# Optimization experiments

Hardware: AMD Instinct MI355X
Metric: run time of the kernel (lower is better)

The kernel has to match this reference:

```python
import jax, jax.numpy as jnp
import numpy as np

D_MODEL = 1024
NUM_HEADS = 16

def setup_inputs() -> dict:
    key = jax.random.key(0)
    k1, k2, k3 = jax.random.split(key, 3)
    scale = 1.0 / np.sqrt(D_MODEL)
    x = jax.random.normal(k1, (2, 2048, D_MODEL), dtype=jnp.float32)
    Wqkv = jax.random.normal(k2, (D_MODEL, 3 * D_MODEL), dtype=jnp.float32) * scale
    bqkv = jnp.zeros((3 * D_MODEL,), dtype=jnp.float32)
    Wout = jax.random.normal(k3, (D_MODEL, D_MODEL), dtype=jnp.float32) * scale
    bout = jnp.zeros((D_MODEL,), dtype=jnp.float32)
    return {"x": x, "Wqkv": Wqkv, "bqkv": bqkv, "Wout": Wout, "bout": bout}

def reference(x, Wqkv, bqkv, Wout, bout):
    B, T, d_model = x.shape
    H = NUM_HEADS
    d_k = d_model // H
    qkv = x @ Wqkv + bqkv                         # [B, T, 3*d_model]
    q, k, v = jnp.split(qkv, 3, axis=-1)
    def reshape(t):
        return t.reshape(B, T, H, d_k).transpose(0, 2, 1, 3)  # [B, H, T, d_k]
    q, k, v = map(reshape, (q, k, v))
    scores = jnp.einsum("bhqd,bhkd->bhqk", q, k) / jnp.sqrt(jnp.float32(d_k))
    attn = jax.nn.softmax(scores, axis=-1)        # [B, H, T, T]
    out = jnp.einsum("bhqk,bhkd->bhqd", attn, v)  # [B, H, T, d_k]
    out = out.transpose(0, 2, 1, 3).reshape(B, T, d_model)
    return out @ Wout + bout
```

## Files before the change

kernel.cpp:

```cpp
#include <hip/hip_runtime.h>
#include <stdint.h>

#define D_MODEL 1024
#define T_SEQ   2048
#define BATCH   2
#define NHEAD   16
#define DK      64

typedef short s16x8 __attribute__((ext_vector_type(8)));
typedef float f32x4 __attribute__((ext_vector_type(4)));
typedef float f32x16 __attribute__((ext_vector_type(16)));

#define MFMA16(a, b, c) __builtin_amdgcn_mfma_f32_16x16x32_bf16((a), (b), (c), 0, 0, 0)
#define MFMA32(a, b, c) __builtin_amdgcn_mfma_f32_32x32x16_bf16((a), (b), (c), 0, 0, 0)
#define CROW(r) ((((r) & 3)) + 8 * ((r) >> 2))

__device__ __forceinline__ unsigned short f2bf(float f) {
    union { float f; unsigned u; } v; v.f = f;
    unsigned r = v.u + 0x7fffu + ((v.u >> 16) & 1u);
    return (unsigned short)(r >> 16);
}

__device__ __forceinline__ unsigned cvtpk_bf16(float lo, float hi) {
    unsigned r;
    asm("v_cvt_pk_bf16_f32 %0, %1, %2" : "=v"(r) : "v"(lo), "v"(hi));
    return r;
}

__device__ __forceinline__ float exp2a(float x) {
    float r;
    asm("v_exp_f32 %0, %1" : "=v"(r) : "v"(x));
    return r;
}

__device__ __forceinline__ float bperm_f(int srclane, float v) {
    int iv = __builtin_bit_cast(int, v);
    int r = __builtin_amdgcn_ds_bpermute(srclane << 2, iv);
    return __builtin_bit_cast(float, r);
}

__global__ __launch_bounds__(256) void cast_x(const float* __restrict__ in,
                                              unsigned short* __restrict__ out, int n8) {
    int i = blockIdx.x * 256 + threadIdx.x;
    if (i >= n8) return;
    const float4* p = reinterpret_cast<const float4*>(in) + (size_t)i * 2;
    float4 a = p[0], b = p[1];
    union { s16x8 v; unsigned short u[8]; } o;
    o.u[0] = f2bf(a.x); o.u[1] = f2bf(a.y); o.u[2] = f2bf(a.z); o.u[3] = f2bf(a.w);
    o.u[4] = f2bf(b.x); o.u[5] = f2bf(b.y); o.u[6] = f2bf(b.z); o.u[7] = f2bf(b.w);
    reinterpret_cast<s16x8*>(out)[i] = o.v;
}

__global__ __launch_bounds__(256) void transpose_cast(const float* __restrict__ in,
                                                      unsigned short* __restrict__ out,
                                                      int R, int C) {
    __shared__ unsigned short tile[64][66];
    int c0 = blockIdx.x * 64, r0 = blockIdx.y * 64;
    int tid = threadIdx.x;
#pragma unroll
    for (int i = 0; i < 16; ++i) {
        int idx = tid + i * 256;
        int r = idx >> 6, c = idx & 63;
        tile[r][c] = f2bf(in[(size_t)(r0 + r) * C + c0 + c]);
    }
    __syncthreads();
#pragma unroll
    for (int i = 0; i < 16; ++i) {
        int idx = tid + i * 256;
        int cc = idx >> 6, rr = idx & 63;
        out[(size_t)(c0 + cc) * R + r0 + rr] = tile[rr][cc];
    }
}

__global__ __launch_bounds__(256) void transpose_v(const unsigned short* __restrict__ in,
                                                   unsigned short* __restrict__ out) {
    __shared__ unsigned short tile[64][66];
    int t0 = blockIdx.x * 64, bh = blockIdx.y;
    int tid = threadIdx.x;
    const unsigned short* src = in + (size_t)bh * T_SEQ * DK;
    unsigned short* dst = out + (size_t)bh * DK * T_SEQ;
#pragma unroll
    for (int i = 0; i < 16; ++i) {
        int idx = tid + i * 256;
        int tr = idx >> 6, d = idx & 63;
        tile[tr][d] = src[(size_t)(t0 + tr) * DK + d];
    }
    __syncthreads();
#pragma unroll
    for (int i = 0; i < 16; ++i) {
        int idx = tid + i * 256;
        int dd = idx >> 6, tt = idx & 63;
        dst[(size_t)dd * T_SEQ + t0 + tt] = tile[tt][dd];
    }
}

__device__ __forceinline__ void gload_lds16(const void* g, void* l) {
    __builtin_amdgcn_global_load_lds(
        (const __attribute__((address_space(1))) void*)g,
        (__attribute__((address_space(3))) void*)l, 16, 0, 0);
}

template <int EPI>
__global__ __launch_bounds__(256) void gemm_bt(
    const unsigned short* __restrict__ A, const unsigned short* __restrict__ Bt,
    int K, int N, const float* __restrict__ bias,
    float* __restrict__ outF,
    unsigned short* __restrict__ Qw, unsigned short* __restrict__ Kw,
    unsigned short* __restrict__ Vw) {
    __shared__ __align__(16) unsigned short lds[2][8192];
    const int tid = threadIdx.x;
    const int lane = tid & 63, wid = tid >> 6;
    const int g = lane >> 4, l15 = lane & 15;
    const int wm = wid >> 1, wn = wid & 1;
    const int mTile = blockIdx.y, nTile = blockIdx.x;
    const unsigned short* Ab = A + (size_t)mTile * 128 * K;
    const unsigned short* Bb = Bt + (size_t)nTile * 128 * K;
    const int srow = tid >> 2, schunk = (tid & 3) * 8;
    f32x4 acc[4][4] = {};

    auto stage = [&](int buf, int kt) {
        const unsigned short* ga = Ab + (size_t)srow * K + kt * 32 + schunk;
        const unsigned short* gb = Bb + (size_t)srow * K + kt * 32 + schunk;
        unsigned short* la = &lds[buf][tid * 8];
        unsigned short* lb = &lds[buf][4096 + tid * 8];
        gload_lds16(ga, la);
        gload_lds16(ga + (size_t)64 * K, la + 2048);
        gload_lds16(gb, lb);
        gload_lds16(gb + (size_t)64 * K, lb + 2048);
    };

    stage(0, 0);
    __syncthreads();
    const int nk = K >> 5;
    int buf = 0;
    for (int kt = 0; kt < nk; ++kt) {
        if (kt + 1 < nk) stage(buf ^ 1, kt + 1);
        const unsigned short* la = &lds[buf][0];
        const unsigned short* lb = &lds[buf][4096];
        s16x8 af[4], bfr[4];
#pragma unroll
        for (int m = 0; m < 4; ++m)
            af[m] = *(const s16x8*)&la[(wm * 64 + m * 16 + l15) * 32 + g * 8];
#pragma unroll
        for (int n = 0; n < 4; ++n)
            bfr[n] = *(const s16x8*)&lb[(wn * 64 + n * 16 + l15) * 32 + g * 8];
#pragma unroll
        for (int m = 0; m < 4; ++m)
#pragma unroll
            for (int n = 0; n < 4; ++n)
                acc[m][n] = MFMA16(af[m], bfr[n], acc[m][n]);
        __syncthreads();
        buf ^= 1;
    }

    const int rowBase = mTile * 128 + wm * 64;
    const int colBase = nTile * 128 + wn * 64;
#pragma unroll
    for (int m = 0; m < 4; ++m) {
#pragma unroll
        for (int n = 0; n < 4; ++n) {
            int col = colBase + n * 16 + l15;
            float bv = bias[col];
#pragma unroll
            for (int r = 0; r < 4; ++r) {
                int row = rowBase + m * 16 + 4 * g + r;
                float val = acc[m][n][r] + bv;
                if (EPI == 1) {
                    outF[(size_t)row * N + col] = val;
                } else {
                    int b = row >> 11, t = row & 2047;
                    if (col < 1024) {
                        int h = col >> 6, d = col & 63;
                        Qw[(((size_t)(b * NHEAD + h)) * T_SEQ + t) * DK + d] =
                            f2bf(val * 0.1803368801111137f);
                    } else if (col < 2048) {
                        int h = (col - 1024) >> 6, d = col & 63;
                        Kw[(((size_t)(b * NHEAD + h)) * T_SEQ + t) * DK + d] = f2bf(val);
                    } else {
                        int h = (col - 2048) >> 6, d = col & 63;
                        Vw[(((size_t)(b * NHEAD + h)) * T_SEQ + t) * DK + d] = f2bf(val);
                    }
                }
            }
        }
    }
}

struct KV {
    s16x8 kf[2][4];
    s16x8 vf[2][4];
};

__global__ __launch_bounds__(256, 2) void attn_fwd(
    const unsigned short* __restrict__ Q, const unsigned short* __restrict__ Kx,
    const unsigned short* __restrict__ Vt, unsigned short* __restrict__ O) {
    const int tid = threadIdx.x;
    const int lane = tid & 63, wid = tid >> 6;
    const int l31 = lane & 31, hi = lane >> 5;
    const int bh = blockIdx.y;
    const int b = bh >> 4, h = bh & 15;
    const int q0 = blockIdx.x * 128 + wid * 32;
    const unsigned short* Qh = Q + (size_t)bh * T_SEQ * DK;
    const unsigned short* Kh = Kx + (size_t)bh * T_SEQ * DK;
    const unsigned short* Vh = Vt + (size_t)bh * DK * T_SEQ;

    s16x8 qf[4];
#pragma unroll
    for (int dt = 0; dt < 4; ++dt)
        qf[dt] = *(const s16x8*)&Qh[(size_t)(q0 + l31) * DK + dt * 16 + hi * 8];

    f32x16 o0 = {}, o1 = {};
    float m = -1e30f, lr = 0.f;

    auto loadKV = [&](int kv0) -> KV {
        KV kv;
#pragma unroll
        for (int kt = 0; kt < 2; ++kt)
#pragma unroll
            for (int dt = 0; dt < 4; ++dt)
                kv.kf[kt][dt] = *(const s16x8*)&Kh[(size_t)(kv0 + kt * 32 + l31) * DK + dt * 16 + hi * 8];
#pragma unroll
        for (int dt2 = 0; dt2 < 2; ++dt2)
#pragma unroll
            for (int ks = 0; ks < 4; ++ks)
                kv.vf[dt2][ks] = *(const s16x8*)&Vh[(size_t)(dt2 * 32 + l31) * T_SEQ + kv0 + ks * 16 + hi * 8];
        return kv;
    };

    auto computeTile = [&](const KV& kv) {
        f32x16 p[2] = {};
#pragma unroll
        for (int kt = 0; kt < 2; ++kt)
#pragma unroll
            for (int dt = 0; dt < 4; ++dt)
                p[kt] = MFMA32(kv.kf[kt][dt], qf[dt], p[kt]);

        float t16[16];
#pragma unroll
        for (int r = 0; r < 16; ++r) t16[r] = fmaxf(p[0][r], p[1][r]);
#pragma unroll
        for (int r = 0; r < 8; ++r) t16[r] = fmaxf(t16[r], t16[r + 8]);
#pragma unroll
        for (int r = 0; r < 4; ++r) t16[r] = fmaxf(t16[r], t16[r + 4]);
        float tm = fmaxf(fmaxf(t16[0], t16[1]), fmaxf(t16[2], t16[3]));
        tm = fmaxf(tm, __shfl_xor(tm, 32));

        if (!__all(tm <= m + 8.0f)) {
            float mn = fmaxf(m, tm);
            float sf = exp2a(m - mn);
            lr *= sf;
            m = mn;
#pragma unroll
            for (int r = 0; r < 16; ++r) {
                float sfr = bperm_f(CROW(r) + 4 * hi, sf);
                o0[r] *= sfr; o1[r] *= sfr;
            }
        }

        float ts0 = 0.f, ts1 = 0.f, ts2 = 0.f, ts3 = 0.f;
#pragma unroll
        for (int kt = 0; kt < 2; ++kt)
#pragma unroll
            for (int r = 0; r < 16; ++r) {
                float e = exp2a(p[kt][r] - m);
                p[kt][r] = e;
                if ((r & 3) == 0) ts0 += e;
                else if ((r & 3) == 1) ts1 += e;
                else if ((r & 3) == 2) ts2 += e;
                else ts3 += e;
            }
        lr += (ts0 + ts1) + (ts2 + ts3);

#pragma unroll
        for (int ks = 0; ks < 4; ++ks) {
            const int kt = ks >> 1, rb = (ks & 1) * 8;
            unsigned w0 = cvtpk_bf16(p[kt][rb + 0], p[kt][rb + 1]);
            unsigned w2 = cvtpk_bf16(p[kt][rb + 4], p[kt][rb + 5]);
            asm volatile("v_permlane32_swap_b32 %0, %1" : "+v"(w0), "+v"(w2));
            unsigned w1 = cvtpk_bf16(p[kt][rb + 2], p[kt][rb + 3]);
            unsigned w3 = cvtpk_bf16(p[kt][rb + 6], p[kt][rb + 7]);
            asm volatile("v_permlane32_swap_b32 %0, %1" : "+v"(w1), "+v"(w3));
            union { unsigned w[4]; s16x8 v; } pu;
            pu.w[0] = w0; pu.w[1] = w1; pu.w[2] = w2; pu.w[3] = w3;
            o0 = MFMA32(pu.v, kv.vf[0][ks], o0);
            o1 = MFMA32(pu.v, kv.vf[1][ks], o1);
        }
    };

    KV bufA = loadKV(0);
#pragma unroll 1
    for (int i = 0; i < 16; ++i) {
        KV bufB = loadKV((2 * i + 1) * 64);
        computeTile(bufA);
        bufA = loadKV(((2 * i + 2) & 31) * 64);
        computeTile(bufB);
    }

    lr += __shfl_xor(lr, 32);
    float li = 1.f / lr;
#pragma unroll
    for (int r = 0; r < 16; ++r) {
        float lir = bperm_f(CROW(r) + 4 * hi, li);
        int q = q0 + CROW(r) + 4 * hi;
        size_t base = ((size_t)(b * T_SEQ + q)) * D_MODEL + h * DK;
        O[base + l31]      = f2bf(o0[r] * lir);
        O[base + 32 + l31] = f2bf(o1[r] * lir);
    }
}

extern "C" void kernel_launch(void* const* d_in, const int* in_sizes, int n_in,
                              void* d_out, int out_size, void* d_ws, size_t ws_size,
                              hipStream_t stream) {
    const float* x    = (const float*)d_in[0];
    const float* Wqkv = (const float*)d_in[1];
    const float* bqkv = (const float*)d_in[2];
    const float* Wout = (const float*)d_in[3];
    const float* bout = (const float*)d_in[4];
    float* out = (float*)d_out;

    char* ws = (char*)d_ws;
    unsigned short* Xbf    = (unsigned short*)(ws + 0);
    unsigned short* WqkvT  = (unsigned short*)(ws + 8388608);
    unsigned short* WoutT  = (unsigned short*)(ws + 14680064);
    unsigned short* Qw     = (unsigned short*)(ws + 16777216);
    unsigned short* Kw     = (unsigned short*)(ws + 25165824);
    unsigned short* Vtmp   = (unsigned short*)(ws + 33554432);
    unsigned short* Vte    = (unsigned short*)(ws + 41943040);
    unsigned short* Ows    = (unsigned short*)(ws + 50331648);

    cast_x<<<2048, 256, 0, stream>>>(x, Xbf, (BATCH * T_SEQ * D_MODEL) / 8);
    transpose_cast<<<dim3(48, 16), 256, 0, stream>>>(Wqkv, WqkvT, 1024, 3072);
    transpose_cast<<<dim3(16, 16), 256, 0, stream>>>(Wout, WoutT, 1024, 1024);
    gemm_bt<0><<<dim3(24, 32), 256, 0, stream>>>(Xbf, WqkvT, 1024, 3072, bqkv,
                                                 nullptr, Qw, Kw, Vtmp);
    transpose_v<<<dim3(32, 32), 256, 0, stream>>>(Vtmp, Vte);
    attn_fwd<<<dim3(16, 32), 256, 0, stream>>>(Qw, Kw, Vte, Ows);
    gemm_bt<1><<<dim3(8, 32), 256, 0, stream>>>(Ows, WoutT, 1024, 1024, bout,
                                                out, nullptr, nullptr, nullptr);
}
```

Before: 270.3 us.

## Split attention KV range across two wave groups and merge partials via LDS

The attention kernel now launches 512 threads per block, with two groups of four waves each handling half of the key/value sequence for the same query rows. The second half writes its partial output, running max and sum to shared memory, and the first half merges them with log-sum-exp rescaling before storing. This doubles the waves per query tile to expose more parallelism and latency hiding, and it drops the explicit double-buffered register prefetch of K/V tiles. It adds a block barrier, about 35 KB of LDS per block and a combine step, and launch bounds now ask for 4 blocks of 512 threads, which tightens the per-thread register budget.

```diff
diff --git a/kernel.cpp b/kernel.cpp
--- a/kernel.cpp
+++ b/kernel.cpp
@@ -191,15 +191,17 @@
     s16x8 vf[2][4];
 };
 
-__global__ __launch_bounds__(256, 2) void attn_fwd(
+__global__ __launch_bounds__(512, 4) void attn_fwd(
     const unsigned short* __restrict__ Q, const unsigned short* __restrict__ Kx,
     const unsigned short* __restrict__ Vt, unsigned short* __restrict__ O) {
+    __shared__ float cls[4][64][34];
     const int tid = threadIdx.x;
     const int lane = tid & 63, wid = tid >> 6;
+    const int qw = wid & 3, half = wid >> 2;
     const int l31 = lane & 31, hi = lane >> 5;
     const int bh = blockIdx.y;
     const int b = bh >> 4, h = bh & 15;
-    const int q0 = blockIdx.x * 128 + wid * 32;
+    const int q0 = blockIdx.x * 128 + qw * 32;
     const unsigned short* Qh = Q + (size_t)bh * T_SEQ * DK;
     const unsigned short* Kh = Kx + (size_t)bh * T_SEQ * DK;
     const unsigned short* Vh = Vt + (size_t)bh * DK * T_SEQ;
@@ -212,7 +214,8 @@
     f32x16 o0 = {}, o1 = {};
     float m = -1e30f, lr = 0.f;
 
-    auto loadKV = [&](int kv0) -> KV {
+    const int kvBase = half * (T_SEQ / 2);
+    for (int kv0 = kvBase; kv0 < kvBase + T_SEQ / 2; kv0 += 64) {
         KV kv;
 #pragma unroll
         for (int kt = 0; kt < 2; ++kt)
@@ -224,10 +227,7 @@
 #pragma unroll
             for (int ks = 0; ks < 4; ++ks)
                 kv.vf[dt2][ks] = *(const s16x8*)&Vh[(size_t)(dt2 * 32 + l31) * T_SEQ + kv0 + ks * 16 + hi * 8];
-        return kv;
-    };
-
-    auto computeTile = [&](const KV& kv) {
+
         f32x16 p[2] = {};
 #pragma unroll
         for (int kt = 0; kt < 2; ++kt)
@@ -285,26 +285,34 @@
             o0 = MFMA32(pu.v, kv.vf[0][ks], o0);
             o1 = MFMA32(pu.v, kv.vf[1][ks], o1);
         }
-    };
-
-    KV bufA = loadKV(0);
-#pragma unroll 1
-    for (int i = 0; i < 16; ++i) {
-        KV bufB = loadKV((2 * i + 1) * 64);
-        computeTile(bufA);
-        bufA = loadKV(((2 * i + 2) & 31) * 64);
-        computeTile(bufB);
     }
 
     lr += __shfl_xor(lr, 32);
-    float li = 1.f / lr;
-#pragma unroll
-    for (int r = 0; r < 16; ++r) {
-        float lir = bperm_f(CROW(r) + 4 * hi, li);
-        int q = q0 + CROW(r) + 4 * hi;
-        size_t base = ((size_t)(b * T_SEQ + q)) * D_MODEL + h * DK;
-        O[base + l31]      = f2bf(o0[r] * lir);
-        O[base + 32 + l31] = f2bf(o1[r] * lir);
+
+    if (half == 1) {
+        float* dst = &cls[qw][lane][0];
+#pragma unroll
+        for (int r = 0; r < 16; ++r) { dst[r] = o0[r]; dst[16 + r] = o1[r]; }
+        dst[32] = m; dst[33] = lr;
+    }
+    __syncthreads();
+    if (half == 0) {
+        const float* src = &cls[qw][lane][0];
+        float m_b = src[32], lr_b = src[33];
+        float mm = fmaxf(m, m_b);
+        float a  = exp2a(m - mm);
+        float bs = exp2a(m_b - mm);
+        float li = 1.f / (lr * a + lr_b * bs);
+        float sa = a * li, sb = bs * li;
+#pragma unroll
+        for (int r = 0; r < 16; ++r) {
+            float sar = bperm_f(CROW(r) + 4 * hi, sa);
+            float sbr = bperm_f(CROW(r) + 4 * hi, sb);
+            int q = q0 + CROW(r) + 4 * hi;
+            size_t base = ((size_t)(b * T_SEQ + q)) * D_MODEL + h * DK;
+            O[base + l31]      = f2bf(o0[r] * sar + src[r] * sbr);
+            O[base + 32 + l31] = f2bf(o1[r] * sar + src[16 + r] * sbr);
+        }
     }
 }
 
@@ -334,7 +342,7 @@
     gemm_bt<0><<<dim3(24, 32), 256, 0, stream>>>(Xbf, WqkvT, 1024, 3072, bqkv,
                                                  nullptr, Qw, Kw, Vtmp);
     transpose_v<<<dim3(32, 32), 256, 0, stream>>>(Vtmp, Vte);
-    attn_fwd<<<dim3(16, 32), 256, 0, stream>>>(Qw, Kw, Vte, Ows);
+    attn_fwd<<<dim3(16, 32), 512, 0, stream>>>(Qw, Kw, Vte, Ows);
     gemm_bt<1><<<dim3(8, 32), 256, 0, stream>>>(Ows, WoutT, 1024, 1024, bout,
                                                 out, nullptr, nullptr, nullptr);
 }
```

New measurement: 322.5 us. +19.3%, slower.
